# Optimization experiments

Hardware: AMD Instinct MI355X
Metric: run time of the kernel (lower is better)

The kernel has to match this reference:

```python
import jax, jax.numpy as jnp
import numpy as np

B, T, E, H = 1, 4096, 768, 12
DH = E // H


def setup_inputs() -> dict:
    key = jax.random.key(0)
    ks = jax.random.split(key, 10)
    s = 0.02
    inp = {
        "queries": jax.random.normal(ks[0], (B, T, E), jnp.float32),
        "values": jax.random.normal(ks[1], (B, T, E), jnp.float32),
        # causal mask (1 = keep, 0 = masked), matches masked_fill(mask == 0, -1e9)
        "mask": jnp.tril(jnp.ones((T, T), jnp.int32))[None, None, :, :],
        "Wq": jax.random.normal(ks[2], (E, E), jnp.float32) * s,
        "bq": jnp.zeros((E,), jnp.float32),
        "Wk": jax.random.normal(ks[3], (E, E), jnp.float32) * s,
        "bk": jnp.zeros((E,), jnp.float32),
        "Wv": jax.random.normal(ks[4], (E, E), jnp.float32) * s,
        "bv": jnp.zeros((E,), jnp.float32),
        "Wo": jax.random.normal(ks[5], (E, E), jnp.float32) * s,
        "bo": jnp.zeros((E,), jnp.float32),
    }
    return inp


def _split_heads(x):
    # [B,T,E] -> [B,H,T,DH]
    return x.reshape(B, T, H, DH).transpose(0, 2, 1, 3)


def reference(queries, values, mask, Wq, bq, Wk, bk, Wv, bv, Wo, bo):
    # torch nn.Linear: y = x @ W.T + b
    q = _split_heads(queries @ Wq.T + bq)
    k = _split_heads(values @ Wk.T + bk)
    v = _split_heads(values @ Wv.T + bv)
    scale = 1.0 / np.sqrt(DH).astype(np.float32)
    logits = jnp.einsum("bhqd,bhkd->bhqk", q, k) * scale  # [B,H,T,T]
    logits = jnp.where(mask == 0, jnp.float32(-1e9), logits)
    probs = jax.nn.softmax(logits, axis=-1)
    ctx = jnp.einsum("bhqk,bhkd->bhqd", probs, v)  # [B,H,T,DH]
    ctx = ctx.transpose(0, 2, 1, 3).reshape(B, T, E)
    return ctx @ Wo.T + bo
```

## Files before the change

### kernel.cpp

```cpp
#include <hip/hip_runtime.h>
#include <hip/hip_bf16.h>


typedef __hip_bfloat16 bf16;
typedef __attribute__((ext_vector_type(8))) short short8;
typedef __attribute__((ext_vector_type(4))) short short4v;
typedef __attribute__((ext_vector_type(4))) float f32x4;

#define TSEQ 4096
#define NHEAD 12
#define DHEAD 64
#define EMB 768

#if defined(__HIP_DEVICE_COMPILE__)
#define MFMA16(a, b, c) __builtin_amdgcn_mfma_f32_16x16x16bf16_1k(a, b, c, 0, 0, 0)
#else
#define MFMA16(a, b, c) (c)
#endif

typedef const __attribute__((address_space(1))) unsigned int* gptr_t;
typedef __attribute__((address_space(3))) unsigned int* lptr_t;

__device__ __forceinline__ void load_lds16(const void* g, void* l) {
    __builtin_amdgcn_global_load_lds((gptr_t)g, (lptr_t)l, 16, 0, 0);
}

__device__ __forceinline__ float b2f(short s) {
    unsigned u = ((unsigned)(unsigned short)s) << 16;
    float f;
    __builtin_memcpy(&f, &u, 4);
    return f;
}

__device__ __forceinline__ short f2bs(float f) {
    bf16 h = __float2bfloat16(f);
    short s;
    __builtin_memcpy(&s, &h, 2);
    return s;
}

struct CvtJob { const float* src; bf16* dst; int n; };
struct CvtArgs { CvtJob j[6]; };

__global__ __launch_bounds__(256) void cvt_kernel(CvtArgs a) {
    const CvtJob jb = a.j[blockIdx.y];
    const int i = (blockIdx.x * 256 + threadIdx.x) * 8;
    if (i >= jb.n) return;
    const float4 x0 = *(const float4*)(jb.src + i);
    const float4 x1 = *(const float4*)(jb.src + i + 4);
    bf16 tmp[8];
    tmp[0] = __float2bfloat16(x0.x); tmp[1] = __float2bfloat16(x0.y);
    tmp[2] = __float2bfloat16(x0.z); tmp[3] = __float2bfloat16(x0.w);
    tmp[4] = __float2bfloat16(x1.x); tmp[5] = __float2bfloat16(x1.y);
    tmp[6] = __float2bfloat16(x1.z); tmp[7] = __float2bfloat16(x1.w);
    *(short8*)(jb.dst + i) = *(const short8*)tmp;
}

template<int NF>
__device__ __forceinline__ void gemm_t(
    const bf16* __restrict__ A, const bf16* __restrict__ W,
    const float* __restrict__ bias,
    bf16* __restrict__ outb, float* __restrict__ outf,
    const int mode, const float scale, const int m0, const int n0,
    bf16* sA, bf16* sB)
{
    const int tid  = threadIdx.x;
    const int lane = tid & 63;
    const int wave = tid >> 6;
    const int wr = wave >> 1, wc = wave & 1;
    const int lg = lane >> 4, lr = lane & 15;

    f32x4 acc[4][NF];
#pragma unroll
    for (int m = 0; m < 4; ++m)
#pragma unroll
        for (int n = 0; n < NF; ++n)
            acc[m][n] = (f32x4){0.f, 0.f, 0.f, 0.f};

    for (int k0 = 0; k0 < EMB; k0 += 64) {
        if (k0) __syncthreads();
#pragma unroll
        for (int is = 0; is < 4; ++is) {
            const int chunk = is * 256 + tid;
            const int row = chunk >> 3;
            const int csw = (chunk & 7) ^ (row & 7);
            load_lds16(A + (size_t)(m0 + row) * EMB + k0 + csw * 8,
                       sA + is * 2048 + wave * 512);
        }
#pragma unroll
        for (int is = 0; is < NF; ++is) {
            const int chunk = is * 256 + tid;
            const int row = chunk >> 3;
            const int csw = (chunk & 7) ^ (row & 7);
            load_lds16(W + (size_t)(n0 + row) * EMB + k0 + csw * 8,
                       sB + is * 2048 + wave * 512);
        }
        __syncthreads();

        short8 af[4][2], bfv[NF][2];
#pragma unroll
        for (int m = 0; m < 4; ++m)
#pragma unroll
            for (int kk = 0; kk < 2; ++kk) {
                const int row = wr * 64 + m * 16 + lr;
                const int cc = (kk * 4 + lg) ^ (row & 7);
                af[m][kk] = *(const short8*)(sA + row * 64 + cc * 8);
            }
#pragma unroll
        for (int n = 0; n < NF; ++n)
#pragma unroll
            for (int kk = 0; kk < 2; ++kk) {
                const int row = wc * (NF * 16) + n * 16 + lr;
                const int cc = (kk * 4 + lg) ^ (row & 7);
                bfv[n][kk] = *(const short8*)(sB + row * 64 + cc * 8);
            }
#pragma unroll
        for (int kk = 0; kk < 2; ++kk)
#pragma unroll
            for (int m = 0; m < 4; ++m)
#pragma unroll
                for (int n = 0; n < NF; ++n)
                    acc[m][n] = __builtin_amdgcn_mfma_f32_16x16x32_bf16(
                        af[m][kk], bfv[n][kk], acc[m][n], 0, 0, 0);
    }

#pragma unroll
    for (int n = 0; n < NF; ++n) {
        const int o = n0 + wc * (NF * 16) + n * 16 + lr;
        const float bv = bias[o];
#pragma unroll
        for (int m = 0; m < 4; ++m) {
            const int tbase = m0 + wr * 64 + m * 16 + lg * 4;
#pragma unroll
            for (int r = 0; r < 4; ++r) {
                const float v = (acc[m][n][r] + bv) * scale;
                const int t = tbase + r;
                if (mode == 0)
                    outb[(size_t)(o >> 6) * TSEQ * DHEAD + (size_t)t * DHEAD + (o & 63)] =
                        __float2bfloat16(v);
                else if (mode == 1)
                    outb[(size_t)(o >> 6) * DHEAD * TSEQ + (size_t)(o & 63) * TSEQ + t] =
                        __float2bfloat16(v);
                else
                    outf[(size_t)t * EMB + o] = v;
            }
        }
    }
}

struct QkvArgs {
    const bf16 *xq, *xv, *Wq, *Wk, *Wv;
    const float *bq, *bk, *bv;
    bf16 *qo, *ko, *vto;
};

__global__ __launch_bounds__(256) void qkv_gemm(QkvArgs a) {
    __shared__ __attribute__((aligned(16))) bf16 sA[128 * 64];
    __shared__ __attribute__((aligned(16))) bf16 sB[128 * 64];
    const int z = blockIdx.z;
    const bf16* A = (z == 0) ? a.xq : a.xv;
    const bf16* W = (z == 0) ? a.Wq : (z == 1 ? a.Wk : a.Wv);
    const float* b = (z == 0) ? a.bq : (z == 1 ? a.bk : a.bv);
    bf16* o = (z == 0) ? a.qo : (z == 1 ? a.ko : a.vto);
    const int mode = (z == 2) ? 1 : 0;
    const float scale = (z == 0) ? 0.18033688011112042f : 1.0f;
    gemm_t<4>(A, W, b, o, nullptr, mode, scale, blockIdx.x * 128, blockIdx.y * 128, sA, sB);
}

__global__ __launch_bounds__(256) void out_gemm(
    const bf16* __restrict__ ctx, const bf16* __restrict__ Wo,
    const float* __restrict__ bo, float* __restrict__ out)
{
    __shared__ __attribute__((aligned(16))) bf16 sA[128 * 64];
    __shared__ __attribute__((aligned(16))) bf16 sB[64 * 64];
    gemm_t<2>(ctx, Wo, bo, nullptr, out, 2, 1.0f, blockIdx.x * 128, blockIdx.y * 64, sA, sB);
}

struct AttnState {
    f32x4 O[4];
    float m, l;
};

__device__ __forceinline__ void stage_tile(
    const bf16* __restrict__ Kh, const bf16* __restrict__ Vh,
    bf16* sK, bf16* sV, const int kv0, const int tid)
{
    const int wave = tid >> 6;
#pragma unroll
    for (int is = 0; is < 2; ++is) {
        const int chunk = is * 256 + tid;
        const int row = chunk >> 3;
        const int csw = (chunk & 7) ^ (row & 7);
        load_lds16(Kh + (size_t)(kv0 + row) * DHEAD + csw * 8,
                   sK + is * 2048 + wave * 512);
        load_lds16(Vh + (size_t)row * TSEQ + kv0 + csw * 8,
                   sV + is * 2048 + wave * 512);
    }
}

template<int BUF>
__device__ __forceinline__ void attn_tile(
    const bf16* kp0, const bf16* kp1,
    const bf16* vp0, const bf16* vp1, const bf16* vp2, const bf16* vp3,
    const short8 (&qf)[2], AttnState& st,
    const int kv0, const int qw, const int lane)
{
    const int lg = lane >> 4, lr = lane & 15;
    if (kv0 > qw + 15) return;

    f32x4 s[4];
    short8 kf[4][2];
#pragma unroll
    for (int n = 0; n < 4; ++n) {
        kf[n][0] = *(const short8*)(kp0 + BUF * 4096 + n * 1024);
        kf[n][1] = *(const short8*)(kp1 + BUF * 4096 + n * 1024);
    }
#pragma unroll
    for (int n = 0; n < 4; ++n) s[n] = (f32x4){0.f, 0.f, 0.f, 0.f};
#pragma unroll
    for (int kk = 0; kk < 2; ++kk)
#pragma unroll
        for (int n = 0; n < 4; ++n)
            s[n] = __builtin_amdgcn_mfma_f32_16x16x32_bf16(
                kf[n][kk], qf[kk], s[n], 0, 0, 0);

    if (kv0 + 63 > qw) {
        const int qi = qw + lr;
#pragma unroll
        for (int n = 0; n < 4; ++n) {
            const int kb = kv0 + n * 16 + lg * 4;
#pragma unroll
            for (int r = 0; r < 4; ++r)
                if (kb + r > qi) s[n][r] = -3.0e38f;
        }
    }

    const float a0 = fmaxf(fmaxf(s[0][0], s[0][1]), fmaxf(s[0][2], s[0][3]));
    const float a1 = fmaxf(fmaxf(s[1][0], s[1][1]), fmaxf(s[1][2], s[1][3]));
    const float a2 = fmaxf(fmaxf(s[2][0], s[2][1]), fmaxf(s[2][2], s[2][3]));
    const float a3 = fmaxf(fmaxf(s[3][0], s[3][1]), fmaxf(s[3][2], s[3][3]));
    float mx = fmaxf(fmaxf(a0, a1), fmaxf(a2, a3));
    mx = fmaxf(mx, __shfl_xor(mx, 16));
    mx = fmaxf(mx, __shfl_xor(mx, 32));

    const float mn = fmaxf(st.m, mx);
    const float al = __builtin_amdgcn_exp2f(st.m - mn);
    st.m = mn;

    float rsn[4];
    short4v pq[4];
#pragma unroll
    for (int n = 0; n < 4; ++n) {
        const float p0 = __builtin_amdgcn_exp2f(s[n][0] - mn);
        const float p1 = __builtin_amdgcn_exp2f(s[n][1] - mn);
        const float p2 = __builtin_amdgcn_exp2f(s[n][2] - mn);
        const float p3 = __builtin_amdgcn_exp2f(s[n][3] - mn);
        rsn[n] = (p0 + p1) + (p2 + p3);
        pq[n][0] = f2bs(p0); pq[n][1] = f2bs(p1);
        pq[n][2] = f2bs(p2); pq[n][3] = f2bs(p3);
    }
    float rs = (rsn[0] + rsn[1]) + (rsn[2] + rsn[3]);
    rs += __shfl_xor(rs, 16);
    rs += __shfl_xor(rs, 32);
    st.l = st.l * al + rs;

#pragma unroll
    for (int nd = 0; nd < 4; ++nd)
#pragma unroll
        for (int r = 0; r < 4; ++r)
            st.O[nd][r] *= al;

#pragma unroll
    for (int nd = 0; nd < 4; ++nd) {
        f32x4 o = st.O[nd];
        o = MFMA16(*(const short4v*)(vp0 + BUF * 4096 + nd * 1024), pq[0], o);
        o = MFMA16(*(const short4v*)(vp1 + BUF * 4096 + nd * 1024), pq[1], o);
        o = MFMA16(*(const short4v*)(vp2 + BUF * 4096 + nd * 1024), pq[2], o);
        o = MFMA16(*(const short4v*)(vp3 + BUF * 4096 + nd * 1024), pq[3], o);
        st.O[nd] = o;
    }
}

__global__ __launch_bounds__(256, 4) void attn_kernel(
    const bf16* __restrict__ Q, const bf16* __restrict__ K,
    const bf16* __restrict__ VT, bf16* __restrict__ Opart,
    float* __restrict__ ml, const int nch_max, const int U)
{
    __shared__ __attribute__((aligned(16))) bf16 sK[2][64 * 64];
    __shared__ __attribute__((aligned(16))) bf16 sV[2][64 * 64];

    const int tid  = threadIdx.x;
    const int lane = tid & 63;
    const int wave = tid >> 6;
    const int lg = lane >> 4, lr = lane & 15;

    const int bid = blockIdx.x;
    const int h = bid % 12;
    int rem = (U - 1) - (bid / 12);
    int g = 0;
    while (g < 7) {
        const int cap = (g + 1 < nch_max) ? g + 1 : nch_max;
        const int gu = 8 * cap;
        if (rem < gu) break;
        rem -= gu;
        ++g;
    }
    const int d = (g + 1 < nch_max) ? g + 1 : nch_max;
    const int bx = 8 * g + rem / d;
    const int c = rem % d;

    const int q0 = bx * 64;
    const int qw = q0 + wave * 16;
    const int S = bx + 1;
    const int t0 = (c * S) / d;
    const int t1 = ((c + 1) * S) / d;

    const bf16* Qh = Q  + (size_t)h * TSEQ * DHEAD;
    const bf16* Kh = K  + (size_t)h * TSEQ * DHEAD;
    const bf16* Vh = VT + (size_t)h * DHEAD * TSEQ;

    short8 qf[2];
#pragma unroll
    for (int kk = 0; kk < 2; ++kk)
        qf[kk] = *(const short8*)(Qh + (size_t)(qw + lr) * DHEAD + kk * 32 + lg * 8);

    const int kb0 = lr * 64 + ((lg ^ (lr & 7)) * 8);
    const bf16* kp0 = &sK[0][0] + kb0;
    const bf16* kp1 = &sK[0][0] + (kb0 ^ 32);
    const int vx = ((lg >> 1) ^ (lr & 7)) * 8;
    const int vb = lr * 64 + (lg & 1) * 4;
    const bf16* vp0 = &sV[0][0] + vb + (0 ^ vx);
    const bf16* vp1 = &sV[0][0] + vb + (16 ^ vx);
    const bf16* vp2 = &sV[0][0] + vb + (32 ^ vx);
    const bf16* vp3 = &sV[0][0] + vb + (48 ^ vx);

    AttnState st;
#pragma unroll
    for (int nd = 0; nd < 4; ++nd) st.O[nd] = (f32x4){0.f, 0.f, 0.f, 0.f};
    st.m = -3.0e38f; st.l = 0.f;

    stage_tile(Kh, Vh, &sK[0][0], &sV[0][0], t0 * 64, tid);
    __syncthreads();

    int it = t0;
    while (it < t1) {
        if (it + 1 < t1) stage_tile(Kh, Vh, &sK[1][0], &sV[1][0], (it + 1) * 64, tid);
        attn_tile<0>(kp0, kp1, vp0, vp1, vp2, vp3, qf, st, it * 64, qw, lane);
        __syncthreads();
        ++it;
        if (it >= t1) break;
        if (it + 1 < t1) stage_tile(Kh, Vh, &sK[0][0], &sV[0][0], (it + 1) * 64, tid);
        attn_tile<1>(kp0, kp1, vp0, vp1, vp2, vp3, qf, st, it * 64, qw, lane);
        __syncthreads();
        ++it;
    }

    const int u = (h * 64 + bx) * nch_max + c;
    bf16* op = Opart + (size_t)u * 4096;
    float* mlp = ml + (size_t)u * 128;
    const int q = wave * 16 + lr;
#pragma unroll
    for (int nd = 0; nd < 4; ++nd) {
        short4v ov;
        ov[0] = f2bs(st.O[nd][0]); ov[1] = f2bs(st.O[nd][1]);
        ov[2] = f2bs(st.O[nd][2]); ov[3] = f2bs(st.O[nd][3]);
        *(short4v*)(op + q * 64 + nd * 16 + lg * 4) = ov;
    }
    if (lg == 0) {
        mlp[q] = st.m;
        mlp[64 + q] = st.l;
    }
}

__global__ __launch_bounds__(256) void combine_kernel(
    const bf16* __restrict__ Opart, const float* __restrict__ ml,
    bf16* __restrict__ ctx, const int nch_max)
{
    const int h  = blockIdx.y;
    const int bx = blockIdx.x;
    const int tid = threadIdx.x;
    const int row = tid >> 2;
    const int dp  = (tid & 3) * 16;
    const int ub = (h * 64 + bx) * nch_max;
    const int g = bx >> 3;
    const int nchb = (nch_max > 1) ? ((g + 1 < nch_max) ? g + 1 : nch_max) : 1;

    float M = -3.0e38f;
    for (int c = 0; c < nchb; ++c)
        M = fmaxf(M, ml[(size_t)(ub + c) * 128 + row]);

    float L = 0.f;
    float acc[16];
#pragma unroll
    for (int i = 0; i < 16; ++i) acc[i] = 0.f;
    for (int c = 0; c < nchb; ++c) {
        const float mc = ml[(size_t)(ub + c) * 128 + row];
        const float lc = ml[(size_t)(ub + c) * 128 + 64 + row];
        const float w = __builtin_amdgcn_exp2f(mc - M);
        L += lc * w;
        const bf16* op = Opart + ((size_t)(ub + c) * 64 + row) * 64 + dp;
        const short8 v0 = *(const short8*)op;
        const short8 v1 = *(const short8*)(op + 8);
#pragma unroll
        for (int i = 0; i < 8; ++i) acc[i] += w * b2f(v0[i]);
#pragma unroll
        for (int i = 0; i < 8; ++i) acc[8 + i] += w * b2f(v1[i]);
    }
    const float invL = 1.0f / L;

    bf16 outv[16];
#pragma unroll
    for (int i = 0; i < 16; ++i) outv[i] = __float2bfloat16(acc[i] * invL);
    const int t = bx * 64 + row;
    bf16* dst = ctx + (size_t)t * EMB + h * DHEAD + dp;
    *(short8*)dst = *(const short8*)outv;
    *(short8*)(dst + 8) = *(const short8*)(outv + 8);
}

extern "C" void kernel_launch(void* const* d_in, const int* in_sizes, int n_in,
                              void* d_out, int out_size, void* d_ws, size_t ws_size,
                              hipStream_t stream) {
    const float* queries = (const float*)d_in[0];
    const float* values  = (const float*)d_in[1];
    const float* Wq = (const float*)d_in[3];
    const float* bq = (const float*)d_in[4];
    const float* Wk = (const float*)d_in[5];
    const float* bk = (const float*)d_in[6];
    const float* Wv = (const float*)d_in[7];
    const float* bv = (const float*)d_in[8];
    const float* Wo = (const float*)d_in[9];
    const float* bo = (const float*)d_in[10];
    float* out = (float*)d_out;

    const size_t NTE = (size_t)TSEQ * EMB;
    const size_t WSZ = (size_t)EMB * EMB;
    bf16* ws  = (bf16*)d_ws;
    bf16* qb  = ws;
    bf16* vb  = qb + NTE;
    bf16* wqb = vb + NTE;
    bf16* wkb = wqb + WSZ;
    bf16* wvb = wkb + WSZ;
    bf16* wob = wvb + WSZ;
    bf16* qh  = wob + WSZ;
    bf16* kh  = qh + NTE;
    bf16* vth = kh + NTE;
    bf16* ctx = qb;

    const size_t fixed_elems = 5 * NTE + 4 * WSZ;
    int nch = 8;
    for (;;) {
        const size_t units = (size_t)NHEAD * (TSEQ / 64) * nch;
        const size_t need = fixed_elems * 2 + units * 4096 * 2 + units * 128 * 4;
        if (ws_size >= need || nch == 1) break;
        nch = (nch == 8) ? 4 : 1;
    }
    const size_t units = (size_t)NHEAD * (TSEQ / 64) * nch;
    bf16* opart = ws + fixed_elems;
    float* ml = (float*)(opart + units * 4096);

    int U = 0;
    for (int g = 0; g < 8; ++g) U += 8 * ((g + 1 < nch) ? g + 1 : nch);

    CvtArgs ca;
    ca.j[0] = {queries, qb,  (int)NTE};
    ca.j[1] = {values,  vb,  (int)NTE};
    ca.j[2] = {Wq,      wqb, (int)WSZ};
    ca.j[3] = {Wk,      wkb, (int)WSZ};
    ca.j[4] = {Wv,      wvb, (int)WSZ};
    ca.j[5] = {Wo,      wob, (int)WSZ};
    cvt_kernel<<<dim3((NTE + 2047) / 2048, 6), 256, 0, stream>>>(ca);

    QkvArgs a{qb, vb, wqb, wkb, wvb, bq, bk, bv, qh, kh, vth};
    qkv_gemm<<<dim3(TSEQ / 128, EMB / 128, 3), 256, 0, stream>>>(a);
    attn_kernel<<<dim3(12 * U), 256, 0, stream>>>(qh, kh, vth, opart, ml, nch, U);
    combine_kernel<<<dim3(TSEQ / 64, NHEAD), 256, 0, stream>>>(opart, ml, ctx, nch);
    out_gemm<<<dim3(TSEQ / 128, EMB / 64), 256, 0, stream>>>(ctx, wob, bo, out);
}
```

Before: 115.0 us.

## Remap GEMM blocks for XCD-local reuse and skip softmax rescale

The QKV and output GEMMs now use a flattened 1D grid whose block index is remapped so blocks on the same XCD (index mod 8) share column tiles, aiming for better L2 reuse of weight/activation tiles across the chiplets. Separately, the attention online softmax defers updating the running max unless the new max exceeds it by more than 8 (in log2 units), so the per-tile rescaling of O and l is skipped in the common case. This trades exact max tracking for bounded exponent growth (p up to 2^8), which is safe in fp32 but could slightly affect bf16 precision of P.

```diff
diff --git a/kernel.cpp b/kernel.cpp
--- a/kernel.cpp
+++ b/kernel.cpp
@@ -157,14 +157,20 @@
 __global__ __launch_bounds__(256) void qkv_gemm(QkvArgs a) {
     __shared__ __attribute__((aligned(16))) bf16 sA[128 * 64];
     __shared__ __attribute__((aligned(16))) bf16 sB[128 * 64];
-    const int z = blockIdx.z;
+    const int z = blockIdx.y;
+    const int b = blockIdx.x;
+    const int xcd = b & 7;
+    const int rest = b >> 3;
+    const int cc = rest % 6;
+    const int rg = rest / 6;
+    const int rr = xcd + 8 * rg;
     const bf16* A = (z == 0) ? a.xq : a.xv;
     const bf16* W = (z == 0) ? a.Wq : (z == 1 ? a.Wk : a.Wv);
-    const float* b = (z == 0) ? a.bq : (z == 1 ? a.bk : a.bv);
+    const float* bias = (z == 0) ? a.bq : (z == 1 ? a.bk : a.bv);
     bf16* o = (z == 0) ? a.qo : (z == 1 ? a.ko : a.vto);
     const int mode = (z == 2) ? 1 : 0;
     const float scale = (z == 0) ? 0.18033688011112042f : 1.0f;
-    gemm_t<4>(A, W, b, o, nullptr, mode, scale, blockIdx.x * 128, blockIdx.y * 128, sA, sB);
+    gemm_t<4>(A, W, bias, o, nullptr, mode, scale, rr * 128, cc * 128, sA, sB);
 }
 
 __global__ __launch_bounds__(256) void out_gemm(
@@ -173,7 +179,13 @@
 {
     __shared__ __attribute__((aligned(16))) bf16 sA[128 * 64];
     __shared__ __attribute__((aligned(16))) bf16 sB[64 * 64];
-    gemm_t<2>(ctx, Wo, bo, nullptr, out, 2, 1.0f, blockIdx.x * 128, blockIdx.y * 64, sA, sB);
+    const int b = blockIdx.x;
+    const int xcd = b & 7;
+    const int rest = b >> 3;
+    const int cc = rest % 12;
+    const int rg = rest / 12;
+    const int rr = xcd + 8 * rg;
+    gemm_t<2>(ctx, Wo, bo, nullptr, out, 2, 1.0f, rr * 128, cc * 64, sA, sB);
 }
 
 struct AttnState {
@@ -243,18 +255,29 @@
     mx = fmaxf(mx, __shfl_xor(mx, 16));
     mx = fmaxf(mx, __shfl_xor(mx, 32));
 
-    const float mn = fmaxf(st.m, mx);
-    const float al = __builtin_amdgcn_exp2f(st.m - mn);
-    st.m = mn;
+    float mref;
+    if (__all(mx <= st.m + 8.0f)) {
+        mref = st.m;
+    } else {
+        mref = fmaxf(st.m, mx);
+        const float al = __builtin_amdgcn_exp2f(st.m - mref);
+        st.m = mref;
+        st.l *= al;
+#pragma unroll
+        for (int nd = 0; nd < 4; ++nd)
+#pragma unroll
+            for (int r = 0; r < 4; ++r)
+                st.O[nd][r] *= al;
+    }
 
     float rsn[4];
     short4v pq[4];
 #pragma unroll
     for (int n = 0; n < 4; ++n) {
-        const float p0 = __builtin_amdgcn_exp2f(s[n][0] - mn);
-        const float p1 = __builtin_amdgcn_exp2f(s[n][1] - mn);
-        const float p2 = __builtin_amdgcn_exp2f(s[n][2] - mn);
-        const float p3 = __builtin_amdgcn_exp2f(s[n][3] - mn);
+        const float p0 = __builtin_amdgcn_exp2f(s[n][0] - mref);
+        const float p1 = __builtin_amdgcn_exp2f(s[n][1] - mref);
+        const float p2 = __builtin_amdgcn_exp2f(s[n][2] - mref);
+        const float p3 = __builtin_amdgcn_exp2f(s[n][3] - mref);
         rsn[n] = (p0 + p1) + (p2 + p3);
         pq[n][0] = f2bs(p0); pq[n][1] = f2bs(p1);
         pq[n][2] = f2bs(p2); pq[n][3] = f2bs(p3);
@@ -262,13 +285,7 @@
     float rs = (rsn[0] + rsn[1]) + (rsn[2] + rsn[3]);
     rs += __shfl_xor(rs, 16);
     rs += __shfl_xor(rs, 32);
-    st.l = st.l * al + rs;
-
-#pragma unroll
-    for (int nd = 0; nd < 4; ++nd)
-#pragma unroll
-        for (int r = 0; r < 4; ++r)
-            st.O[nd][r] *= al;
+    st.l += rs;
 
 #pragma unroll
     for (int nd = 0; nd < 4; ++nd) {
@@ -471,8 +488,8 @@
     cvt_kernel<<<dim3((NTE + 2047) / 2048, 6), 256, 0, stream>>>(ca);
 
     QkvArgs a{qb, vb, wqb, wkb, wvb, bq, bk, bv, qh, kh, vth};
-    qkv_gemm<<<dim3(TSEQ / 128, EMB / 128, 3), 256, 0, stream>>>(a);
+    qkv_gemm<<<dim3(192, 3), 256, 0, stream>>>(a);
     attn_kernel<<<dim3(12 * U), 256, 0, stream>>>(qh, kh, vth, opart, ml, nch, U);
     combine_kernel<<<dim3(TSEQ / 64, NHEAD), 256, 0, stream>>>(opart, ml, ctx, nch);
-    out_gemm<<<dim3(TSEQ / 128, EMB / 64), 256, 0, stream>>>(ctx, wob, bo, out);
-}
+    out_gemm<<<dim3(384), 256, 0, stream>>>(ctx, wob, bo, out);
+}
```

Measured after the change: 114.7 us (median of 3 runs). About the same (-0.3%).
